# Optimization experiments

Hardware: AMD Instinct MI355X
Metric: run time of the kernel (lower is better)

The kernel has to match this reference:

```python
import jax, jax.numpy as jnp
import numpy as np
import math

FD_RADIUS = 2
FD_H = 0.01
GAUSS_WIN = 9
GAUSS_STD = 2.0


def _fd_kernel():
    # 4th-order central FD stencil for 2nd derivative (radius 2), scaled by 1/h^2
    k = np.array([-1/12, 4/3, -5/2, 4/3, -1/12], dtype=np.float32)
    return jnp.asarray(k / FD_H**2)


def _gauss_kernel():
    R = GAUSS_WIN // 2
    xs = np.arange(-R, R + 1, dtype=np.float64)
    c = 1.0 / (GAUSS_STD * math.sqrt(2 * math.pi))
    k = c * np.exp(-xs**2 / (2 * GAUSS_STD**2))
    k = k / k.sum()
    return jnp.asarray(k.astype(np.float32))


def setup_inputs() -> dict:
    key = jax.random.key(0)
    x = jax.random.normal(key, (8, 4, 1048576), dtype=jnp.float32)
    return {"x": x, "fd_kernel": _fd_kernel(), "gauss_kernel": _gauss_kernel()}


def _depthwise_valid(sig, k1d):
    # sig: [B, C, T]; same 1D kernel applied independently to every channel
    C = sig.shape[1]
    w = jnp.tile(k1d.reshape(1, 1, -1), (C, 1, 1))  # [C, 1, K]
    return jax.lax.conv_general_dilated(
        sig, w, window_strides=(1,), padding="VALID",
        dimension_numbers=("NCH", "OIH", "NCH"), feature_group_count=C)


def reference(x, fd_kernel, gauss_kernel):
    # Finite-difference 2nd derivative (valid conv), then Gaussian smoothing (valid conv)
    x_diff = _depthwise_valid(x, fd_kernel)          # [B, C, T-4]
    x_smooth = _depthwise_valid(x_diff, gauss_kernel)  # [B, C, T-12]
    return x_smooth
```

## Files before the change

### kernel.cpp

```cpp
#include <hip/hip_runtime.h>

#define T_IN   1048576
#define T_OUT  1048564
#define ROWS   32
#define QUADS_PER_ROW (T_OUT / 4)
#define TOTAL_QUADS (ROWS * QUADS_PER_ROW)

__global__ __launch_bounds__(256) void pinn_fused_conv13(
    const float* __restrict__ x,
    const float* __restrict__ fd,
    const float* __restrict__ gs,
    float* __restrict__ out)
{
    float f[5], g[9], c[13];
#pragma unroll
    for (int k = 0; k < 13; ++k) c[k] = 0.0f;
#pragma unroll
    for (int i = 0; i < 5; ++i) f[i] = fd[i];
#pragma unroll
    for (int j = 0; j < 9; ++j) g[j] = gs[j];
#pragma unroll
    for (int i = 0; i < 5; ++i)
#pragma unroll
        for (int j = 0; j < 9; ++j) c[i + j] += f[i] * g[j];

    const int stride = gridDim.x * blockDim.x;
    for (int q = blockIdx.x * blockDim.x + threadIdx.x; q < TOTAL_QUADS; q += stride) {
        const int r  = q / QUADS_PER_ROW;
        const int t0 = (q - r * QUADS_PER_ROW) * 4;

        const float* xp = x + (long long)r * T_IN + t0;
        const float4 v0 = *reinterpret_cast<const float4*>(xp);
        const float4 v1 = *reinterpret_cast<const float4*>(xp + 4);
        const float4 v2 = *reinterpret_cast<const float4*>(xp + 8);
        const float4 v3 = *reinterpret_cast<const float4*>(xp + 12);

        float a[16] = {v0.x, v0.y, v0.z, v0.w,
                       v1.x, v1.y, v1.z, v1.w,
                       v2.x, v2.y, v2.z, v2.w,
                       v3.x, v3.y, v3.z, v3.w};

        float o[4];
#pragma unroll
        for (int j = 0; j < 4; ++j) {
            float s = 0.0f;
#pragma unroll
            for (int k = 0; k < 13; ++k) s = fmaf(c[k], a[j + k], s);
            o[j] = s;
        }

        *reinterpret_cast<float4*>(out + (long long)r * T_OUT + t0) =
            make_float4(o[0], o[1], o[2], o[3]);
    }
}

extern "C" void kernel_launch(void* const* d_in, const int* in_sizes, int n_in,
                              void* d_out, int out_size, void* d_ws, size_t ws_size,
                              hipStream_t stream) {
    const float* x  = (const float*)d_in[0];
    const float* fd = (const float*)d_in[1];
    const float* gs = (const float*)d_in[2];
    float* out = (float*)d_out;

    pinn_fused_conv13<<<8192, 256, 0, stream>>>(x, fd, gs, out);
}
```

Baseline: 259.4 us.

## Stage input tiles with halo in LDS and map one block per row segment

New measurement: 221.5 us. 14.6% less time.

```diff
diff --git a/kernel.cpp b/kernel.cpp
--- a/kernel.cpp
+++ b/kernel.cpp
@@ -2,9 +2,8 @@
 
 #define T_IN   1048576
 #define T_OUT  1048564
-#define ROWS   32
-#define QUADS_PER_ROW (T_OUT / 4)
-#define TOTAL_QUADS (ROWS * QUADS_PER_ROW)
+#define QPR    262141
+#define BPR    1024
 
 __global__ __launch_bounds__(256) void pinn_fused_conv13(
     const float* __restrict__ x,
@@ -12,6 +11,24 @@
     const float* __restrict__ gs,
     float* __restrict__ out)
 {
+    __shared__ float lds[1040];
+
+    const int r  = blockIdx.x >> 10;
+    const int b  = blockIdx.x & (BPR - 1);
+    const int t  = threadIdx.x;
+    const int qb = b << 8;
+    const int in0 = qb << 2;
+
+    const float* __restrict__ xrow = x + (size_t)r * T_IN;
+    float* __restrict__ orow = out + (size_t)r * T_OUT;
+
+    const float4 mv = *reinterpret_cast<const float4*>(xrow + in0 + 4 * t);
+    float4 hv = make_float4(0.f, 0.f, 0.f, 0.f);
+    const bool is_halo = (t < 4);
+    if (is_halo && (in0 + 1024 + 4 * t + 4 <= T_IN)) {
+        hv = *reinterpret_cast<const float4*>(xrow + in0 + 1024 + 4 * t);
+    }
+
     float f[5], g[9], c[13];
 #pragma unroll
     for (int k = 0; k < 13; ++k) c[k] = 0.0f;
@@ -22,24 +39,22 @@
 #pragma unroll
     for (int i = 0; i < 5; ++i)
 #pragma unroll
-        for (int j = 0; j < 9; ++j) c[i + j] += f[i] * g[j];
+        for (int j = 0; j < 9; ++j) c[i + j] = fmaf(f[i], g[j], c[i + j]);
 
-    const int stride = gridDim.x * blockDim.x;
-    for (int q = blockIdx.x * blockDim.x + threadIdx.x; q < TOTAL_QUADS; q += stride) {
-        const int r  = q / QUADS_PER_ROW;
-        const int t0 = (q - r * QUADS_PER_ROW) * 4;
+    *reinterpret_cast<float4*>(lds + 4 * t) = mv;
+    if (is_halo) *reinterpret_cast<float4*>(lds + 1024 + 4 * t) = hv;
+    __syncthreads();
 
-        const float* xp = x + (long long)r * T_IN + t0;
-        const float4 v0 = *reinterpret_cast<const float4*>(xp);
-        const float4 v1 = *reinterpret_cast<const float4*>(xp + 4);
-        const float4 v2 = *reinterpret_cast<const float4*>(xp + 8);
-        const float4 v3 = *reinterpret_cast<const float4*>(xp + 12);
+    const int q = qb + t;
+    if (q < QPR) {
+        const float4 w1 = *reinterpret_cast<const float4*>(lds + 4 * t + 4);
+        const float4 w2 = *reinterpret_cast<const float4*>(lds + 4 * t + 8);
+        const float4 w3 = *reinterpret_cast<const float4*>(lds + 4 * t + 12);
 
-        float a[16] = {v0.x, v0.y, v0.z, v0.w,
-                       v1.x, v1.y, v1.z, v1.w,
-                       v2.x, v2.y, v2.z, v2.w,
-                       v3.x, v3.y, v3.z, v3.w};
-
+        const float a[16] = {mv.x, mv.y, mv.z, mv.w,
+                             w1.x, w1.y, w1.z, w1.w,
+                             w2.x, w2.y, w2.z, w2.w,
+                             w3.x, w3.y, w3.z, w3.w};
         float o[4];
 #pragma unroll
         for (int j = 0; j < 4; ++j) {
@@ -48,8 +63,7 @@
             for (int k = 0; k < 13; ++k) s = fmaf(c[k], a[j + k], s);
             o[j] = s;
         }
-
-        *reinterpret_cast<float4*>(out + (long long)r * T_OUT + t0) =
+        *reinterpret_cast<float4*>(orow + 4 * q) =
             make_float4(o[0], o[1], o[2], o[3]);
     }
 }
@@ -62,5 +76,5 @@
     const float* gs = (const float*)d_in[2];
     float* out = (float*)d_out;
 
-    pinn_fused_conv13<<<8192, 256, 0, stream>>>(x, fd, gs, out);
+    pinn_fused_conv13<<<32 * BPR, 256, 0, stream>>>(x, fd, gs, out);
 }
```
